# Performance work log

Measured on AMD Instinct MI355X. Metric: run time of the kernel, lower is better.

Reference implementation:

```python
import jax, jax.numpy as jnp
import numpy as np

N = 50000
E = 600000
IN_DIM = 128
HID = 128
HEADS = 4
OUT = HID // HEADS  # per-head out channels
R = 2
LAYERS = 2
NEG_SLOPE = 0.2


def _glorot(key, shape):
    fan_in, fan_out = shape[-2], shape[-1]
    lim = jnp.sqrt(6.0 / (fan_in + fan_out))
    return jax.random.uniform(key, shape, jnp.float32, -lim, lim)


def setup_inputs() -> dict:
    key = jax.random.key(0)
    ks = jax.random.split(key, 20)
    x = jax.random.normal(ks[0], (N, IN_DIM), jnp.float32)
    eidx = jax.random.randint(ks[1], (2, E), 0, N, jnp.int64 if jax.config.jax_enable_x64 else jnp.int32)
    etype = jax.random.randint(ks[2], (E,), 0, R, eidx.dtype)
    d = IN_DIM
    params = {}
    ki = 3
    for l in range(LAYERS):
        params[f"W{l}"] = _glorot(ks[ki], (R, d, HID)); ki += 1            # per-relation weight
        params[f"Q{l}"] = _glorot(ks[ki], (HID, HEADS)); ki += 1           # query proj (dim=1)
        params[f"K{l}"] = _glorot(ks[ki], (HID, HEADS)); ki += 1           # key proj
        params[f"cb{l}"] = jnp.zeros((HID,), jnp.float32)                   # conv bias
        params[f"pW{l}"] = _glorot(ks[ki], (HID, HID)); ki += 1            # proj Linear weight [out,in]
        params[f"pb{l}"] = jnp.zeros((HID,), jnp.float32)
        d = HID
    return dict(x=x, eidx=eidx, etype=etype, **params)


def _rgat_conv(h, src, dst, etype, W, Q, K, b):
    # per-relation transform of all nodes: [R, N, HID]
    xw = jnp.einsum('ni,rio->rno', h, W)
    out_j = xw[etype, src]          # [E, HID] source features under edge's relation
    out_i = xw[etype, dst]          # [E, HID] target features under edge's relation
    # additive self-attention, dim=1: alpha [E, HEADS]
    alpha = jax.nn.leaky_relu(out_i @ Q + out_j @ K, NEG_SLOPE)
    # segment softmax over destination nodes (across-relation)
    m = jax.ops.segment_max(alpha, dst, num_segments=N)
    m = jnp.where(jnp.isfinite(m), m, 0.0)
    e = jnp.exp(alpha - m[dst])
    s = jax.ops.segment_sum(e, dst, num_segments=N)
    a = e / (s[dst] + 1e-16)
    # weighted messages and scatter-sum aggregation
    msg = out_j.reshape(E, HEADS, OUT) * a[:, :, None]
    agg = jax.ops.segment_sum(msg.reshape(E, HID), dst, num_segments=N)
    return agg + b


def reference(x, eidx, etype, W0, Q0, K0, cb0, pW0, pb0, W1, Q1, K1, cb1, pW1, pb1):
    src, dst = eidx[0], eidx[1]  # flow source_to_target: aggregate at eidx[1]
    h = x
    for (W, Q, K, cb, pW, pb) in ((W0, Q0, K0, cb0, pW0, pb0), (W1, Q1, K1, cb1, pW1, pb1)):
        h = _rgat_conv(h, src, dst, etype, W, Q, K, cb)
        h = jax.nn.elu(h @ pW.T + pb)
    return h
```

## Files before the change

kernel.cpp:

```cpp
#include <hip/hip_runtime.h>
#include <hip/hip_bf16.h>

typedef __hip_bfloat16 bf16;
typedef short s16x8 __attribute__((ext_vector_type(8)));
typedef float f32x4 __attribute__((ext_vector_type(4)));

#define N_NODES 50000
#define NPAD    50048
#define E_EDGES 600000
#define HID     128
#define HEADS   4
#define SCAN_B  196

#define GB_IDX  2344
#define GB_XB   3125
#define GB_WT   256
#define GB_QUAD 3125
#define GB_BIG  8824
#define GB_GEMM 1564
#define GB_QK   196

__device__ __forceinline__ unsigned short f2bf_bits(float f) {
  unsigned u = __float_as_uint(f);
  u += 0x7fffu + ((u >> 16) & 1u);
  return (unsigned short)(u >> 16);
}
__device__ __forceinline__ float bf2f(unsigned short b) {
  return __uint_as_float(((unsigned)b) << 16);
}
__device__ __forceinline__ float lo_f(unsigned v) { return __uint_as_float(v << 16); }
__device__ __forceinline__ float hi_f(unsigned v) { return __uint_as_float(v & 0xffff0000u); }
__device__ __forceinline__ float lrelu(float v) { return fmaxf(v, 0.2f * v); }
__device__ __forceinline__ float elu(float v) { return v > 0.f ? v : __expf(v) - 1.f; }

__global__ __launch_bounds__(256) void detect_zero_kernel(const unsigned short* __restrict__ xb,
                                                          const int* __restrict__ ei,
                                                          int* __restrict__ flags,
                                                          int* __restrict__ zp, int nz) {
  int t = threadIdx.x;
  int i = blockIdx.x * 256 + t;
  if (i < nz) zp[i] = 0;
  if (blockIdx.x == 0) {
    __shared__ int cnt[2];
    if (t < 2) cnt[t] = 0;
    __syncthreads();
    unsigned short v = xb[2 * t];
    int ex = (v >> 7) & 0xFF;
    if (ex < 119 || ex > 135) atomicAdd(&cnt[0], 1);
    if (ei[2 * t + 1] != 0) atomicAdd(&cnt[1], 1);
    __syncthreads();
    if (t == 0) {
      flags[0] = (cnt[0] > 64) ? 1 : 0;
      flags[1] = (cnt[1] == 0) ? 1 : 0;
    }
  }
}

struct P8 { const void* src[8]; int dstoff[8]; int n[8]; };
__global__ __launch_bounds__(256) void cvt_all_kernel(const int* __restrict__ eidx,
                                                      const int* __restrict__ etype,
                                                      int* __restrict__ dstA, int* __restrict__ pk,
                                                      int* __restrict__ deg,
                                                      const void* __restrict__ x,
                                                      unsigned short* __restrict__ hb,
                                                      const void* __restrict__ w0,
                                                      const void* __restrict__ w1,
                                                      unsigned short* __restrict__ Wbt,
                                                      P8 tab, float* __restrict__ base,
                                                      const int* __restrict__ flags) {
  const int b = blockIdx.x, t = threadIdx.x;
  if (b < GB_IDX) {
    int e = b * 256 + t;
    if (e >= E_EDGES) return;
    int s, d, r;
    if (flags[1]) {
      const long long* e64 = (const long long*)eidx;
      const long long* t64 = (const long long*)etype;
      s = (int)e64[e]; d = (int)e64[E_EDGES + e]; r = (int)t64[e];
    } else {
      s = eidx[e]; d = eidx[E_EDGES + e]; r = etype[e];
    }
    dstA[e] = d;
    pk[e] = s | (r << 16);
    atomicAdd(&deg[d], 1);
  } else if (b < GB_IDX + GB_XB) {
    int i = (b - GB_IDX) * 256 + t;
    if (flags[0]) {
      const float4* s4 = (const float4*)x;
      float4 a = s4[2 * i], c = s4[2 * i + 1];
      s16x8 o;
      o[0] = (short)f2bf_bits(a.x); o[1] = (short)f2bf_bits(a.y);
      o[2] = (short)f2bf_bits(a.z); o[3] = (short)f2bf_bits(a.w);
      o[4] = (short)f2bf_bits(c.x); o[5] = (short)f2bf_bits(c.y);
      o[6] = (short)f2bf_bits(c.z); o[7] = (short)f2bf_bits(c.w);
      *(s16x8*)(hb + (size_t)i * 8) = o;
    } else {
      *(s16x8*)(hb + (size_t)i * 8) = ((const s16x8*)x)[i];
    }
  } else if (b < GB_IDX + GB_XB + GB_WT) {
    int idx = (b - GB_IDX - GB_XB) * 256 + t;
    int l = idx >> 15, rem = idx & 32767;
    int r = rem >> 14, i = (rem >> 7) & 127, o = rem & 127;
    const void* src = l ? w1 : w0;
    unsigned short v;
    if (flags[0]) v = f2bf_bits(((const float*)src)[rem]);
    else          v = ((const unsigned short*)src)[rem];
    Wbt[(size_t)l * 2 * HID * HID + ((size_t)r * HID + o) * HID + i] = v;
  } else {
    const int f = flags[0];
    int bb = b - GB_IDX - GB_XB - GB_WT;
    for (int k = 0; k < 8; ++k) {
      int n = tab.n[k];
      for (int i = bb * 256 + t; i < n; i += 2 * 256) {
        float v = f ? ((const float*)tab.src[k])[i] : bf2f(((const unsigned short*)tab.src[k])[i]);
        base[tab.dstoff[k] + i] = v;
      }
    }
  }
}

__global__ __launch_bounds__(256) void scan1_bucket_kernel(const int* __restrict__ deg,
                                                           int* __restrict__ excl,
                                                           int* __restrict__ bsum,
                                                           int* __restrict__ bcnt,
                                                           int* __restrict__ nq,
                                                           int* __restrict__ nw) {
  const int b = blockIdx.x, t = threadIdx.x;
  if (b < SCAN_B) {
    __shared__ int sm[256];
    int i = b * 256 + t;
    int v = (i < NPAD) ? deg[i] : 0;
    sm[t] = v;
    __syncthreads();
#pragma unroll
    for (int off = 1; off < 256; off <<= 1) {
      int add = (t >= off) ? sm[t - off] : 0;
      __syncthreads();
      sm[t] += add;
      __syncthreads();
    }
    if (i < NPAD) excl[i] = sm[t] - v;
    if (t == 255) bsum[b] = sm[255];
  } else {
    int n = (b - SCAN_B) * 256 + t;
    int lane = t & 63;
    bool valid = n < N_NODES;
    int d = valid ? deg[n] : 0;
    bool isq = valid && (d <= 16);
    bool isw = valid && (d > 16);
    unsigned long long mq = __ballot(isq);
    unsigned long long mw = __ballot(isw);
    unsigned long long lower = (lane == 63) ? 0x7fffffffffffffffull : ((1ull << lane) - 1ull);
    int baseq = 0, basew = 0;
    int lq = (int)__ffsll(mq) - 1;
    int lw = (int)__ffsll(mw) - 1;
    if (mq && lane == lq) baseq = atomicAdd(&bcnt[0], (int)__popcll(mq));
    if (mw && lane == lw) basew = atomicAdd(&bcnt[1], (int)__popcll(mw));
    if (mq) baseq = __shfl(baseq, lq);
    if (mw) basew = __shfl(basew, lw);
    if (isq) nq[baseq + (int)__popcll(mq & lower)] = n;
    if (isw) nw[basew + (int)__popcll(mw & lower)] = n;
  }
}

__global__ __launch_bounds__(256) void scan23_prep_kernel(const int* __restrict__ excl,
                                                          const int* __restrict__ bsum,
                                                          int* __restrict__ rowstart,
                                                          const unsigned short* __restrict__ Wbt,
                                                          const float* __restrict__ Qf,
                                                          const float* __restrict__ Kf,
                                                          unsigned short* __restrict__ qkt_hi,
                                                          unsigned short* __restrict__ qkt_lo,
                                                          const void* __restrict__ pW0,
                                                          const void* __restrict__ pW1,
                                                          const float* __restrict__ cbf,
                                                          const float* __restrict__ pbf,
                                                          unsigned short* __restrict__ pWTb2,
                                                          float* __restrict__ bo2,
                                                          const int* __restrict__ flags) {
  const int b = blockIdx.x, t = threadIdx.x;
  if (b < SCAN_B) {
    __shared__ int sm[256];
    int v = (t < SCAN_B) ? bsum[t] : 0;
    sm[t] = v;
    __syncthreads();
#pragma unroll
    for (int off = 1; off < 256; off <<= 1) {
      int add = (t >= off) ? sm[t - off] : 0;
      __syncthreads();
      sm[t] += add;
      __syncthreads();
    }
    int bpre = (b > 0) ? sm[b - 1] : 0;
    int i = b * 256 + t;
    if (i < NPAD) rowstart[i] = excl[i] + bpre;
    if (i == 0) rowstart[NPAD] = E_EDGES;
  } else if (b < SCAN_B + 2) {
    int idx = (b - SCAN_B) * 256 + t;
    int i = idx & 127, lr = idx >> 7, l = lr >> 1, r = (lr & 1);
    float aq[4] = {0.f, 0.f, 0.f, 0.f}, ak[4] = {0.f, 0.f, 0.f, 0.f};
    const unsigned short* Wb = Wbt + (size_t)lr * HID * HID;
    const float* Qp = Qf + l * HID * HEADS;
    const float* Kp = Kf + l * HID * HEADS;
    for (int j = 0; j < HID; ++j) {
      float w = bf2f(Wb[j * HID + i]);
      float4 q4 = *(const float4*)(Qp + j * 4);
      float4 k4 = *(const float4*)(Kp + j * 4);
      aq[0] += w * q4.x; aq[1] += w * q4.y; aq[2] += w * q4.z; aq[3] += w * q4.w;
      ak[0] += w * k4.x; ak[1] += w * k4.y; ak[2] += w * k4.z; ak[3] += w * k4.w;
    }
    size_t base = (size_t)l * 16 * HID;
#pragma unroll
    for (int h = 0; h < 4; ++h) {
      unsigned short qh = f2bf_bits(aq[h]);
      unsigned short kh = f2bf_bits(ak[h]);
      float qres = aq[h] - bf2f(qh);
      float kres = ak[h] - bf2f(kh);
      qkt_hi[base + (size_t)(r * 4 + h) * HID + i] = qh;
      qkt_lo[base + (size_t)(r * 4 + h) * HID + i] = f2bf_bits(qres);
      qkt_hi[base + (size_t)(8 + r * 4 + h) * HID + i] = kh;
      qkt_lo[base + (size_t)(8 + r * 4 + h) * HID + i] = f2bf_bits(kres);
    }
  } else {
    const int wave = t >> 6, lane = t & 63;
    int ob = (b - SCAN_B - 2) * 4 + wave;
    int o = ob & 127, l = ob >> 7;
    const void* pWraw = l ? pW1 : pW0;
    const float* cb = cbf + l * HID;
    const int f = flags[0];
    float part = 0.f;
#pragma unroll
    for (int i = lane; i < HID; i += 64) {
      float w = f ? ((const float*)pWraw)[o * HID + i] : bf2f(((const unsigned short*)pWraw)[o * HID + i]);
      pWTb2[(size_t)l * HID * HID + o * HID + i] = f2bf_bits(w);
      part += cb[i] * w;
    }
#pragma unroll
    for (int off = 32; off > 0; off >>= 1) part += __shfl_xor(part, off);
    if (lane == 0) bo2[l * HID + o] = pbf[l * HID + o] + part;
  }
}

__global__ __launch_bounds__(256) void scatter_kernel(const int* __restrict__ dstA,
                                                      const int* __restrict__ pk,
                                                      const int* __restrict__ rowstart,
                                                      int* __restrict__ cnt,
                                                      int* __restrict__ eord) {
  int e = blockIdx.x * 256 + threadIdx.x;
  if (e >= E_EDGES) return;
  int d = dstA[e];
  int pos = rowstart[d] + atomicAdd(&cnt[d], 1);
  eord[pos] = pk[e];
}

__global__ __launch_bounds__(256) void gemm_qk_kernel(const unsigned short* __restrict__ hb,
                                                      const unsigned short* __restrict__ Wbt,
                                                      unsigned short* __restrict__ xw,
                                                      const unsigned short* __restrict__ qkt_hi,
                                                      const unsigned short* __restrict__ qkt_lo,
                                                      float4* __restrict__ qi4,
                                                      float4* __restrict__ kj4) {
  __shared__ unsigned short smem[8704];
  const int t = threadIdx.x;
  const int wave = t >> 6, lane = t & 63;
  const int lm = lane & 15, q = lane >> 4;
  if (blockIdx.x < GB_GEMM) {
    unsigned short (*As)[136] = (unsigned short(*)[136])smem;
    const int row0 = blockIdx.x * 32;
    const int r = wave >> 1, colb = (wave & 1) * 64;
    const unsigned short* Bt = Wbt + (size_t)r * HID * HID;
    s16x8 bfr[4][4];
#pragma unroll
    for (int kc = 0; kc < 4; ++kc) {
      const int ko = kc * 32 + q * 8;
#pragma unroll
      for (int ct = 0; ct < 4; ++ct)
        bfr[kc][ct] = *(const s16x8*)(Bt + (size_t)(colb + ct * 16 + lm) * HID + ko);
    }
    const unsigned short* gsrc = hb + (size_t)row0 * HID;
#pragma unroll
    for (int j = 0; j < 2; ++j) {
      int idx = j * 256 + t;
      *(s16x8*)&As[idx >> 4][(idx & 15) * 8] = *(const s16x8*)(gsrc + idx * 8);
    }
    __syncthreads();
    f32x4 acc[2][4];
#pragma unroll
    for (int a = 0; a < 2; ++a)
#pragma unroll
      for (int c = 0; c < 4; ++c) { f32x4 z = {0.f, 0.f, 0.f, 0.f}; acc[a][c] = z; }
#pragma unroll
    for (int kc = 0; kc < 4; ++kc) {
      const int ko = kc * 32 + q * 8;
#pragma unroll
      for (int rt = 0; rt < 2; ++rt) {
        s16x8 a = *(const s16x8*)&As[rt * 16 + lm][ko];
#pragma unroll
        for (int ct = 0; ct < 4; ++ct)
          acc[rt][ct] = __builtin_amdgcn_mfma_f32_16x16x32_bf16(a, bfr[kc][ct], acc[rt][ct], 0, 0, 0);
      }
    }
    __syncthreads();
#pragma unroll
    for (int rr = 0; rr < 2; ++rr) {
      if (r == rr) {
#pragma unroll
        for (int rt = 0; rt < 2; ++rt)
#pragma unroll
          for (int i = 0; i < 4; ++i) {
            int rloc = rt * 16 + q * 4 + i;
#pragma unroll
            for (int ct = 0; ct < 4; ++ct)
              As[rloc][colb + ct * 16 + lm] = f2bf_bits(acc[rt][ct][i]);
          }
      }
      __syncthreads();
      unsigned short* dst = xw + ((size_t)rr * NPAD + row0) * HID;
#pragma unroll
      for (int j = 0; j < 2; ++j) {
        int idx = j * 256 + t;
        int rw = idx >> 4, cb8 = (idx & 15) * 8;
        if (row0 + rw < N_NODES)
          *(s16x8*)(dst + (size_t)rw * HID + cb8) = *(const s16x8*)&As[rw][cb8];
      }
      __syncthreads();
    }
  } else {
    float (*st)[16][68] = (float(*)[16][68])smem;
    const int row0 = (blockIdx.x - GB_GEMM) * 256 + wave * 64;
    if (row0 < NPAD) {
      s16x8 bhi[4], blo[4], af[4][4];
#pragma unroll
      for (int kc = 0; kc < 4; ++kc) {
        const int ko = kc * 32 + q * 8;
        bhi[kc] = *(const s16x8*)(qkt_hi + (size_t)lm * HID + ko);
        blo[kc] = *(const s16x8*)(qkt_lo + (size_t)lm * HID + ko);
      }
#pragma unroll
      for (int kc = 0; kc < 4; ++kc) {
        const int ko = kc * 32 + q * 8;
#pragma unroll
        for (int rt = 0; rt < 4; ++rt)
          af[kc][rt] = *(const s16x8*)(hb + (size_t)(row0 + rt * 16 + lm) * HID + ko);
      }
      f32x4 acc[4];
#pragma unroll
      for (int a = 0; a < 4; ++a) { f32x4 z = {0.f, 0.f, 0.f, 0.f}; acc[a] = z; }
#pragma unroll
      for (int kc = 0; kc < 4; ++kc)
#pragma unroll
        for (int rt = 0; rt < 4; ++rt) {
          acc[rt] = __builtin_amdgcn_mfma_f32_16x16x32_bf16(af[kc][rt], bhi[kc], acc[rt], 0, 0, 0);
          acc[rt] = __builtin_amdgcn_mfma_f32_16x16x32_bf16(af[kc][rt], blo[kc], acc[rt], 0, 0, 0);
        }
#pragma unroll
      for (int rt = 0; rt < 4; ++rt)
        *(f32x4*)&st[wave][lm][rt * 16 + q * 4] = acc[rt];
    }
    __syncthreads();
    if (row0 < NPAD) {
      int n = row0 + lane;
      if (n < N_NODES) {
        float4 v;
        v.x = st[wave][0][lane]; v.y = st[wave][1][lane]; v.z = st[wave][2][lane]; v.w = st[wave][3][lane];
        qi4[n] = v;
        v.x = st[wave][4][lane]; v.y = st[wave][5][lane]; v.z = st[wave][6][lane]; v.w = st[wave][7][lane];
        qi4[NPAD + n] = v;
        v.x = st[wave][8][lane]; v.y = st[wave][9][lane]; v.z = st[wave][10][lane]; v.w = st[wave][11][lane];
        kj4[n] = v;
        v.x = st[wave][12][lane]; v.y = st[wave][13][lane]; v.z = st[wave][14][lane]; v.w = st[wave][15][lane];
        kj4[NPAD + n] = v;
      }
    }
  }
}

__global__ __launch_bounds__(256) void edge_all_kernel(
    const int* __restrict__ rowstart, const int* __restrict__ eord,
    const float4* __restrict__ qi4, const float4* __restrict__ kj4,
    const unsigned short* __restrict__ xw, unsigned short* __restrict__ aggb,
    const int* __restrict__ nq, const int* __restrict__ nw,
    const int* __restrict__ bcnt) {
  __shared__ volatile float wbuf[1152];
  const int t = threadIdx.x;
  const int wave = t >> 6, lane = t & 63;
  if (blockIdx.x < GB_QUAD) {
    const int g = lane >> 4, li = lane & 15;
    const int idx = blockIdx.x * 16 + wave * 4 + g;
    const int cq = bcnt[0];
    const bool act = idx < cq;
    const int n = act ? nq[idx] : 0;
    const int start = rowstart[n];
    const int dg = act ? (rowstart[n + 1] - start) : 0;
    int p = 0;
    float w0 = 0.f, w1 = 0.f, w2 = 0.f, w3 = 0.f;
    if (li < dg) {
      p = eord[start + li];
      int s = p & 0xffff, r = p >> 16;
      float4 k4 = kj4[r ? (NPAD + s) : s];
      float4 q4 = r ? qi4[NPAD + n] : qi4[n];
      w0 = __expf(fminf(lrelu(q4.x + k4.x), 85.f));
      w1 = __expf(fminf(lrelu(q4.y + k4.y), 85.f));
      w2 = __expf(fminf(lrelu(q4.z + k4.z), 85.f));
      w3 = __expf(fminf(lrelu(q4.w + k4.w), 85.f));
    }
    const int wg = (wave << 2) | g;
    volatile float* wls = &wbuf[wg * 68];
    wls[0 * 17 + li] = w0; wls[1 * 17 + li] = w1;
    wls[2 * 17 + li] = w2; wls[3 * 17 + li] = w3;
    float s0 = w0, s1 = w1, s2 = w2, s3 = w3;
#pragma unroll
    for (int off = 8; off > 0; off >>= 1) {
      s0 += __shfl_xor(s0, off); s1 += __shfl_xor(s1, off);
      s2 += __shfl_xor(s2, off); s3 += __shfl_xor(s3, off);
    }
    const int hh = li >> 2;
    float ssel = hh == 0 ? s0 : hh == 1 ? s1 : hh == 2 ? s2 : s3;
    float a0 = 0.f, a1 = 0.f, a2 = 0.f, a3 = 0.f, a4 = 0.f, a5 = 0.f, a6 = 0.f, a7 = 0.f;
    volatile const float* wrh = &wls[hh * 17];
    const int co = li * 8;
    const int gbase = lane & 48;
#pragma unroll 1
    for (int e0 = 0; e0 < dg; e0 += 4) {
      int pe[4];
      uint4 v[4];
#pragma unroll
      for (int u = 0; u < 4; ++u) {
        int e = e0 + u;
        pe[u] = __shfl(p, gbase + (e < dg ? e : 0));
      }
#pragma unroll
      for (int u = 0; u < 4; ++u)
        v[u] = *(const uint4*)(xw + ((size_t)((pe[u] & 0xffff) + (pe[u] >> 16) * NPAD) << 7) + co);
#pragma unroll
      for (int u = 0; u < 4; ++u) {
        int e = e0 + u;
        float we = (e < dg) ? wrh[e] : 0.f;
        a0 = fmaf(lo_f(v[u].x), we, a0); a1 = fmaf(hi_f(v[u].x), we, a1);
        a2 = fmaf(lo_f(v[u].y), we, a2); a3 = fmaf(hi_f(v[u].y), we, a3);
        a4 = fmaf(lo_f(v[u].z), we, a4); a5 = fmaf(hi_f(v[u].z), we, a5);
        a6 = fmaf(lo_f(v[u].w), we, a6); a7 = fmaf(hi_f(v[u].w), we, a7);
      }
    }
    if (act) {
      float inv = 1.f / (ssel + 1e-16f);
      uint4 o;
      o.x = (unsigned)f2bf_bits(a0 * inv) | ((unsigned)f2bf_bits(a1 * inv) << 16);
      o.y = (unsigned)f2bf_bits(a2 * inv) | ((unsigned)f2bf_bits(a3 * inv) << 16);
      o.z = (unsigned)f2bf_bits(a4 * inv) | ((unsigned)f2bf_bits(a5 * inv) << 16);
      o.w = (unsigned)f2bf_bits(a6 * inv) | ((unsigned)f2bf_bits(a7 * inv) << 16);
      *(uint4*)(aggb + ((size_t)n << 7) + co) = o;
    }
  } else {
    const int idx = (blockIdx.x - GB_QUAD) * 4 + wave;
    const int cw = bcnt[1];
    if (idx >= cw) return;
    const int n = nw[idx];
    unsigned* outp = (unsigned*)(aggb + ((size_t)n << 7)) + lane;
    const int start = rowstart[n];
    const int deg = rowstart[n + 1] - start;
    const int hh = lane >> 4;
    const int ch2 = lane << 1;
    float2 acc = {0.f, 0.f};
    float ssel;
    volatile float* wls = &wbuf[wave * 288];
    if (deg <= 64) {
      int p = 0;
      float w0 = 0.f, w1 = 0.f, w2 = 0.f, w3 = 0.f;
      if (lane < deg) {
        p = eord[start + lane];
        int s = p & 0xffff, r = p >> 16;
        float4 k4 = kj4[r ? (NPAD + s) : s];
        float4 q4 = r ? qi4[NPAD + n] : qi4[n];
        w0 = __expf(fminf(lrelu(q4.x + k4.x), 85.f));
        w1 = __expf(fminf(lrelu(q4.y + k4.y), 85.f));
        w2 = __expf(fminf(lrelu(q4.z + k4.z), 85.f));
        w3 = __expf(fminf(lrelu(q4.w + k4.w), 85.f));
      }
      float s0 = w0, s1 = w1, s2 = w2, s3 = w3;
#pragma unroll
      for (int off = 32; off > 0; off >>= 1) {
        s0 += __shfl_xor(s0, off); s1 += __shfl_xor(s1, off);
        s2 += __shfl_xor(s2, off); s3 += __shfl_xor(s3, off);
      }
      ssel = hh == 0 ? s0 : hh == 1 ? s1 : hh == 2 ? s2 : s3;
      wls[0 * 72 + lane] = w0;
      wls[1 * 72 + lane] = w1;
      wls[2 * 72 + lane] = w2;
      wls[3 * 72 + lane] = w3;
      volatile const float* wrh = &wls[hh * 72];
      const int degp = (deg + 15) & ~15;
#pragma unroll 1
      for (int e = 0; e < degp; e += 16) {
        int pp[16];
        unsigned vv[16];
#pragma unroll
        for (int u = 0; u < 16; ++u)
          pp[u] = __builtin_amdgcn_readlane(p, e + u);
#pragma unroll
        for (int u = 0; u < 16; ++u)
          vv[u] = *(const unsigned*)(xw + ((size_t)((pp[u] & 0xffff) + (pp[u] >> 16) * NPAD) << 7) + ch2);
#pragma unroll
        for (int u = 0; u < 16; ++u) {
          float we = wrh[e + u];
          acc.x = fmaf(lo_f(vv[u]), we, acc.x);
          acc.y = fmaf(hi_f(vv[u]), we, acc.y);
        }
      }
    } else {
      const float4 q0 = qi4[n], q1 = qi4[NPAD + n];
      float4 m = make_float4(-1e30f, -1e30f, -1e30f, -1e30f);
      for (int e = start; e < start + deg; ++e) {
        int pe = eord[e];
        int s = pe & 0xffff, r = pe >> 16;
        float4 k4 = kj4[(size_t)r * NPAD + s];
        float4 q4 = r ? q1 : q0;
        m.x = fmaxf(m.x, lrelu(q4.x + k4.x)); m.y = fmaxf(m.y, lrelu(q4.y + k4.y));
        m.z = fmaxf(m.z, lrelu(q4.z + k4.z)); m.w = fmaxf(m.w, lrelu(q4.w + k4.w));
      }
      float4 sv = make_float4(0.f, 0.f, 0.f, 0.f);
      for (int e = start; e < start + deg; ++e) {
        int pe = eord[e];
        int s = pe & 0xffff, r = pe >> 16;
        float4 k4 = kj4[(size_t)r * NPAD + s];
        float4 q4 = r ? q1 : q0;
        float w0 = __expf(lrelu(q4.x + k4.x) - m.x);
        float w1 = __expf(lrelu(q4.y + k4.y) - m.y);
        float w2 = __expf(lrelu(q4.z + k4.z) - m.z);
        float w3 = __expf(lrelu(q4.w + k4.w) - m.w);
        sv.x += w0; sv.y += w1; sv.z += w2; sv.w += w3;
        float we = hh == 0 ? w0 : hh == 1 ? w1 : hh == 2 ? w2 : w3;
        unsigned v = *(const unsigned*)(xw + (((size_t)r * NPAD + s) << 7) + ch2);
        acc.x = fmaf(lo_f(v), we, acc.x);
        acc.y = fmaf(hi_f(v), we, acc.y);
      }
      ssel = hh == 0 ? sv.x : hh == 1 ? sv.y : hh == 2 ? sv.z : sv.w;
    }
    float inv = 1.f / (ssel + 1e-16f);
    *outp = (unsigned)f2bf_bits(acc.x * inv) | ((unsigned)f2bf_bits(acc.y * inv) << 16);
  }
}

__global__ __launch_bounds__(256) void proj_mfma(const unsigned short* __restrict__ aggb,
                                                 const unsigned short* __restrict__ pWTb,
                                                 const float* __restrict__ bo,
                                                 unsigned short* __restrict__ hbout,
                                                 void* __restrict__ dout,
                                                 const int* __restrict__ flags) {
  __shared__ unsigned short As[64][136];
  const int t = threadIdx.x;
  const int wave = t >> 6, lane = t & 63;
  const int row0 = blockIdx.x * 64;
  const int h = wave >> 1;
  const int colb = (wave & 1) * 64;
  const int lm = lane & 15, q = lane >> 4;
  s16x8 bfr[4][4];
#pragma unroll
  for (int kc = 0; kc < 4; ++kc) {
    const int ko = kc * 32 + q * 8;
#pragma unroll
    for (int ct = 0; ct < 4; ++ct)
      bfr[kc][ct] = *(const s16x8*)(pWTb + (size_t)(colb + ct * 16 + lm) * HID + ko);
  }
  const unsigned short* gsrc = aggb + (size_t)row0 * HID;
#pragma unroll
  for (int j = 0; j < 4; ++j) {
    int idx = j * 256 + t;
    *(s16x8*)&As[idx >> 4][(idx & 15) * 8] = *(const s16x8*)(gsrc + idx * 8);
  }
  __syncthreads();
  f32x4 acc[2][4];
#pragma unroll
  for (int a = 0; a < 2; ++a)
#pragma unroll
    for (int c = 0; c < 4; ++c) { f32x4 z = {0.f, 0.f, 0.f, 0.f}; acc[a][c] = z; }
#pragma unroll
  for (int kc = 0; kc < 4; ++kc) {
    const int ko = kc * 32 + q * 8;
#pragma unroll
    for (int rt = 0; rt < 2; ++rt) {
      s16x8 a = *(const s16x8*)&As[(2 * h + rt) * 16 + lm][ko];
#pragma unroll
      for (int ct = 0; ct < 4; ++ct)
        acc[rt][ct] = __builtin_amdgcn_mfma_f32_16x16x32_bf16(a, bfr[kc][ct], acc[rt][ct], 0, 0, 0);
    }
  }
  __syncthreads();
  const int f32final = (dout != nullptr) && flags[0];
  if (!f32final) {
    unsigned short* dstp = dout ? (unsigned short*)dout : hbout;
#pragma unroll
    for (int rt = 0; rt < 2; ++rt)
#pragma unroll
      for (int i = 0; i < 4; ++i) {
        int rloc = (2 * h + rt) * 16 + q * 4 + i;
#pragma unroll
        for (int ct = 0; ct < 4; ++ct) {
          int o = colb + ct * 16 + lm;
          float v = elu(acc[rt][ct][i] + bo[o]);
          As[rloc][o] = f2bf_bits(v);
        }
      }
    __syncthreads();
#pragma unroll
    for (int j = 0; j < 4; ++j) {
      int idx = j * 256 + t;
      int rw = idx >> 4, cb8 = (idx & 15) * 8;
      if (row0 + rw < N_NODES)
        *(s16x8*)(dstp + (size_t)(row0 + rw) * HID + cb8) = *(const s16x8*)&As[rw][cb8];
    }
  } else {
    float* fdst = (float*)dout;
    float (*Fs)[132] = (float(*)[132])&As[0][0];
#pragma unroll
    for (int h2 = 0; h2 < 2; ++h2) {
      if (h == h2) {
#pragma unroll
        for (int rt = 0; rt < 2; ++rt)
#pragma unroll
          for (int i = 0; i < 4; ++i) {
            int rloc = rt * 16 + q * 4 + i;
#pragma unroll
            for (int ct = 0; ct < 4; ++ct) {
              int o = colb + ct * 16 + lm;
              Fs[rloc][o] = elu(acc[rt][ct][i] + bo[o]);
            }
          }
      }
      __syncthreads();
#pragma unroll
      for (int j = 0; j < 4; ++j) {
        int idx = j * 256 + t;
        int rw = idx >> 5, cb4 = (idx & 31) * 4;
        if (row0 + h2 * 32 + rw < N_NODES)
          *(float4*)(fdst + (size_t)(row0 + h2 * 32 + rw) * HID + cb4) = *(const float4*)&Fs[rw][cb4];
      }
      __syncthreads();
    }
  }
}

extern "C" void kernel_launch(void* const* d_in, const int* in_sizes, int n_in,
                              void* d_out, int out_size, void* d_ws, size_t ws_size,
                              hipStream_t stream) {
  const void* x     = d_in[0];
  const int*  eidx  = (const int*)d_in[1];
  const int*  etype = (const int*)d_in[2];
  const int iW[2] = {3, 9}, iQ[2] = {4, 10}, iK[2] = {5, 11}, icb[2] = {6, 12}, ipW[2] = {7, 13}, ipb[2] = {8, 14};

  float* ws = (float*)d_ws;
  size_t off = 0;
  int*   flags = (int*)(ws + off); off += 16;
  unsigned short* hb   = (unsigned short*)(ws + off); off += (size_t)NPAD * HID / 2;
  unsigned short* xw   = (unsigned short*)(ws + off); off += (size_t)NPAD * HID;
  float* qi   = ws + off; off += (size_t)2 * NPAD * HEADS;
  float* kj   = ws + off; off += (size_t)2 * NPAD * HEADS;
  unsigned short* aggb = (unsigned short*)(ws + off); off += (size_t)NPAD * HID / 2;
  int* dstA = (int*)(ws + off); off += E_EDGES;
  int* pk   = (int*)(ws + off); off += E_EDGES;
  int* eord = (int*)(ws + off); off += E_EDGES;
  int* deg  = (int*)(ws + off); off += NPAD;
  int* cnt  = (int*)(ws + off); off += NPAD;
  int* bcnt = (int*)(ws + off); off += 16;
  int* excl = (int*)(ws + off); off += NPAD;
  int* rowstart = (int*)(ws + off); off += NPAD + 16;
  int* bsum  = (int*)(ws + off); off += 256;
  int* nq   = (int*)(ws + off); off += NPAD;
  int* nwl  = (int*)(ws + off); off += NPAD;
  unsigned short* Wbt   = (unsigned short*)(ws + off); off += (size_t)2 * 2 * HID * HID / 2;
  unsigned short* pWTb2 = (unsigned short*)(ws + off); off += (size_t)2 * HID * HID / 2;
  unsigned short* qkt_hi = (unsigned short*)(ws + off); off += (size_t)2 * 16 * HID / 2;
  unsigned short* qkt_lo = (unsigned short*)(ws + off); off += (size_t)2 * 16 * HID / 2;
  float* Qf  = ws + off; off += 2 * HID * HEADS;
  float* Kf  = ws + off; off += 2 * HID * HEADS;
  float* cbf = ws + off; off += 2 * HID;
  float* pbf = ws + off; off += 2 * HID;
  float* bo2 = ws + off; off += 2 * HID;

  detect_zero_kernel<<<(2 * NPAD + 16 + 255) / 256, 256, 0, stream>>>((const unsigned short*)x, eidx, flags, deg, 2 * NPAD + 16);

  {
    P8 tab;
    float* base = ws;
    for (int l = 0; l < 2; ++l) {
      tab.src[l * 4 + 0] = d_in[iQ[l]];  tab.dstoff[l * 4 + 0] = (int)(Qf - base) + l * HID * HEADS;  tab.n[l * 4 + 0] = HID * HEADS;
      tab.src[l * 4 + 1] = d_in[iK[l]];  tab.dstoff[l * 4 + 1] = (int)(Kf - base) + l * HID * HEADS;  tab.n[l * 4 + 1] = HID * HEADS;
      tab.src[l * 4 + 2] = d_in[icb[l]]; tab.dstoff[l * 4 + 2] = (int)(cbf - base) + l * HID;         tab.n[l * 4 + 2] = HID;
      tab.src[l * 4 + 3] = d_in[ipb[l]]; tab.dstoff[l * 4 + 3] = (int)(pbf - base) + l * HID;         tab.n[l * 4 + 3] = HID;
    }
    cvt_all_kernel<<<GB_IDX + GB_XB + GB_WT + 2, 256, 0, stream>>>(eidx, etype, dstA, pk, deg,
                                                                   x, hb, d_in[iW[0]], d_in[iW[1]], Wbt,
                                                                   tab, ws, flags);
  }

  scan1_bucket_kernel<<<SCAN_B + SCAN_B, 256, 0, stream>>>(deg, excl, bsum, bcnt, nq, nwl);

  scan23_prep_kernel<<<SCAN_B + 2 + 64, 256, 0, stream>>>(excl, bsum, rowstart,
                                                          Wbt, Qf, Kf, qkt_hi, qkt_lo,
                                                          d_in[ipW[0]], d_in[ipW[1]], cbf, pbf, pWTb2, bo2, flags);

  scatter_kernel<<<(E_EDGES + 255) / 256, 256, 0, stream>>>(dstA, pk, rowstart, cnt, eord);

  for (int l = 0; l < 2; ++l) {
    gemm_qk_kernel<<<GB_GEMM + GB_QK, 256, 0, stream>>>(hb, Wbt + (size_t)l * 2 * HID * HID, xw,
                                                        qkt_hi + (size_t)l * 16 * HID, qkt_lo + (size_t)l * 16 * HID,
                                                        (float4*)qi, (float4*)kj);
    edge_all_kernel<<<GB_QUAD + GB_BIG, 256, 0, stream>>>(rowstart, eord, (const float4*)qi, (const float4*)kj,
                                                          xw, aggb, nq, nwl, bcnt);
    proj_mfma<<<NPAD / 64, 256, 0, stream>>>(aggb, pWTb2 + (size_t)l * HID * HID, bo2 + l * HID, hb,
                                             (l == 1) ? d_out : nullptr, flags);
  }
}
```

Baseline: 343.6 us.

## Fuse input conversion and projection into per-layer GEMM+QK kernels

The x-to-bf16 conversion moves out of cvt_all and into a new layer-0 kernel that does the relation GEMM and the Q/K projection from one LDS tile. The layer-0 output projection plus ELU is fused with the layer-1 GEMM and QK, so the intermediate hb buffer is never written to or reread from global memory. The edge kernel's block order is also swapped so the big-node blocks are scheduled first. The goal is fewer launches and less global traffic, at the cost of larger 64-row tiles with two LDS buffers, which may reduce occupancy.

Result: no change. 343.1 us (-0.1%).

```diff
diff --git a/kernel.cpp b/kernel.cpp
--- a/kernel.cpp
+++ b/kernel.cpp
@@ -13,12 +13,9 @@
 #define SCAN_B  196
 
 #define GB_IDX  2344
-#define GB_XB   3125
 #define GB_WT   256
 #define GB_QUAD 3125
 #define GB_BIG  8824
-#define GB_GEMM 1564
-#define GB_QK   196
 
 __device__ __forceinline__ unsigned short f2bf_bits(float f) {
   unsigned u = __float_as_uint(f);
@@ -61,8 +58,6 @@
                                                       const int* __restrict__ etype,
                                                       int* __restrict__ dstA, int* __restrict__ pk,
                                                       int* __restrict__ deg,
-                                                      const void* __restrict__ x,
-                                                      unsigned short* __restrict__ hb,
                                                       const void* __restrict__ w0,
                                                       const void* __restrict__ w1,
                                                       unsigned short* __restrict__ Wbt,
@@ -83,22 +78,8 @@
     dstA[e] = d;
     pk[e] = s | (r << 16);
     atomicAdd(&deg[d], 1);
-  } else if (b < GB_IDX + GB_XB) {
-    int i = (b - GB_IDX) * 256 + t;
-    if (flags[0]) {
-      const float4* s4 = (const float4*)x;
-      float4 a = s4[2 * i], c = s4[2 * i + 1];
-      s16x8 o;
-      o[0] = (short)f2bf_bits(a.x); o[1] = (short)f2bf_bits(a.y);
-      o[2] = (short)f2bf_bits(a.z); o[3] = (short)f2bf_bits(a.w);
-      o[4] = (short)f2bf_bits(c.x); o[5] = (short)f2bf_bits(c.y);
-      o[6] = (short)f2bf_bits(c.z); o[7] = (short)f2bf_bits(c.w);
-      *(s16x8*)(hb + (size_t)i * 8) = o;
-    } else {
-      *(s16x8*)(hb + (size_t)i * 8) = ((const s16x8*)x)[i];
-    }
-  } else if (b < GB_IDX + GB_XB + GB_WT) {
-    int idx = (b - GB_IDX - GB_XB) * 256 + t;
+  } else if (b < GB_IDX + GB_WT) {
+    int idx = (b - GB_IDX) * 256 + t;
     int l = idx >> 15, rem = idx & 32767;
     int r = rem >> 14, i = (rem >> 7) & 127, o = rem & 127;
     const void* src = l ? w1 : w0;
@@ -108,7 +89,7 @@
     Wbt[(size_t)l * 2 * HID * HID + ((size_t)r * HID + o) * HID + i] = v;
   } else {
     const int f = flags[0];
-    int bb = b - GB_IDX - GB_XB - GB_WT;
+    int bb = b - GB_IDX - GB_WT;
     for (int k = 0; k < 8; ++k) {
       int n = tab.n[k];
       for (int i = bb * 256 + t; i < n; i += 2 * 256) {
@@ -253,126 +234,214 @@
   eord[pos] = pk[e];
 }
 
-__global__ __launch_bounds__(256) void gemm_qk_kernel(const unsigned short* __restrict__ hb,
-                                                      const unsigned short* __restrict__ Wbt,
-                                                      unsigned short* __restrict__ xw,
-                                                      const unsigned short* __restrict__ qkt_hi,
-                                                      const unsigned short* __restrict__ qkt_lo,
-                                                      float4* __restrict__ qi4,
-                                                      float4* __restrict__ kj4) {
-  __shared__ unsigned short smem[8704];
+__device__ __forceinline__ void gemm64_from_lds(unsigned short (*As)[136], unsigned short (*Cs)[136],
+                                                const unsigned short* __restrict__ Wbt,
+                                                unsigned short* __restrict__ xw, int row0,
+                                                int wave, int lm, int q, int t) {
+  const int r = wave >> 1, colb = (wave & 1) * 64;
+  const unsigned short* Bt = Wbt + (size_t)r * HID * HID;
+  s16x8 bfr[4][4];
+#pragma unroll
+  for (int kc = 0; kc < 4; ++kc) {
+    const int ko = kc * 32 + q * 8;
+#pragma unroll
+    for (int ct = 0; ct < 4; ++ct)
+      bfr[kc][ct] = *(const s16x8*)(Bt + (size_t)(colb + ct * 16 + lm) * HID + ko);
+  }
+  f32x4 acc[4][4];
+#pragma unroll
+  for (int a = 0; a < 4; ++a)
+#pragma unroll
+    for (int c = 0; c < 4; ++c) { f32x4 z = {0.f, 0.f, 0.f, 0.f}; acc[a][c] = z; }
+#pragma unroll
+  for (int kc = 0; kc < 4; ++kc) {
+    const int ko = kc * 32 + q * 8;
+#pragma unroll
+    for (int rt = 0; rt < 4; ++rt) {
+      s16x8 a = *(const s16x8*)&As[rt * 16 + lm][ko];
+#pragma unroll
+      for (int ct = 0; ct < 4; ++ct)
+        acc[rt][ct] = __builtin_amdgcn_mfma_f32_16x16x32_bf16(a, bfr[kc][ct], acc[rt][ct], 0, 0, 0);
+    }
+  }
+  __syncthreads();
+#pragma unroll
+  for (int rr = 0; rr < 2; ++rr) {
+    if (r == rr) {
+#pragma unroll
+      for (int rt = 0; rt < 4; ++rt)
+#pragma unroll
+        for (int i = 0; i < 4; ++i) {
+          int rloc = rt * 16 + q * 4 + i;
+#pragma unroll
+          for (int ct = 0; ct < 4; ++ct)
+            Cs[rloc][colb + ct * 16 + lm] = f2bf_bits(acc[rt][ct][i]);
+        }
+    }
+    __syncthreads();
+    unsigned short* dst = xw + ((size_t)rr * NPAD + row0) * HID;
+#pragma unroll
+    for (int j = 0; j < 4; ++j) {
+      int idx = j * 256 + t;
+      int rw = idx >> 4, cb8 = (idx & 15) * 8;
+      if (row0 + rw < N_NODES)
+        *(s16x8*)(dst + (size_t)rw * HID + cb8) = *(const s16x8*)&Cs[rw][cb8];
+    }
+    __syncthreads();
+  }
+}
+
+__device__ __forceinline__ void qk16_from_lds(unsigned short (*As)[136], unsigned short (*Cs)[136],
+                                              const unsigned short* __restrict__ qkt_hi,
+                                              const unsigned short* __restrict__ qkt_lo,
+                                              float4* __restrict__ qi4, float4* __restrict__ kj4,
+                                              int row0, int wave, int lane, int lm, int q) {
+  s16x8 bhi[4], blo[4], af[4];
+#pragma unroll
+  for (int kc = 0; kc < 4; ++kc) {
+    const int ko = kc * 32 + q * 8;
+    bhi[kc] = *(const s16x8*)(qkt_hi + (size_t)lm * HID + ko);
+    blo[kc] = *(const s16x8*)(qkt_lo + (size_t)lm * HID + ko);
+    af[kc]  = *(const s16x8*)&As[wave * 16 + lm][ko];
+  }
+  f32x4 acc = {0.f, 0.f, 0.f, 0.f};
+#pragma unroll
+  for (int kc = 0; kc < 4; ++kc) {
+    acc = __builtin_amdgcn_mfma_f32_16x16x32_bf16(af[kc], bhi[kc], acc, 0, 0, 0);
+    acc = __builtin_amdgcn_mfma_f32_16x16x32_bf16(af[kc], blo[kc], acc, 0, 0, 0);
+  }
+  float (*Fs)[16][17] = (float(*)[16][17])&Cs[0][0];
+#pragma unroll
+  for (int i = 0; i < 4; ++i)
+    Fs[wave][lm][q * 4 + i] = acc[i];
+  __syncthreads();
+  if (lane < 16) {
+    int n = row0 + wave * 16 + lane;
+    if (n < N_NODES) {
+      float4 v;
+      v.x = Fs[wave][0][lane];  v.y = Fs[wave][1][lane];  v.z = Fs[wave][2][lane];  v.w = Fs[wave][3][lane];
+      qi4[n] = v;
+      v.x = Fs[wave][4][lane];  v.y = Fs[wave][5][lane];  v.z = Fs[wave][6][lane];  v.w = Fs[wave][7][lane];
+      qi4[NPAD + n] = v;
+      v.x = Fs[wave][8][lane];  v.y = Fs[wave][9][lane];  v.z = Fs[wave][10][lane]; v.w = Fs[wave][11][lane];
+      kj4[n] = v;
+      v.x = Fs[wave][12][lane]; v.y = Fs[wave][13][lane]; v.z = Fs[wave][14][lane]; v.w = Fs[wave][15][lane];
+      kj4[NPAD + n] = v;
+    }
+  }
+}
+
+__global__ __launch_bounds__(256) void fused_l0_kernel(const void* __restrict__ x,
+                                                       const unsigned short* __restrict__ Wbt,
+                                                       unsigned short* __restrict__ xw,
+                                                       const unsigned short* __restrict__ qkt_hi,
+                                                       const unsigned short* __restrict__ qkt_lo,
+                                                       float4* __restrict__ qi4,
+                                                       float4* __restrict__ kj4,
+                                                       const int* __restrict__ flags) {
+  __shared__ unsigned short As[64][136];
+  __shared__ unsigned short Cs[64][136];
   const int t = threadIdx.x;
   const int wave = t >> 6, lane = t & 63;
   const int lm = lane & 15, q = lane >> 4;
-  if (blockIdx.x < GB_GEMM) {
-    unsigned short (*As)[136] = (unsigned short(*)[136])smem;
-    const int row0 = blockIdx.x * 32;
-    const int r = wave >> 1, colb = (wave & 1) * 64;
-    const unsigned short* Bt = Wbt + (size_t)r * HID * HID;
-    s16x8 bfr[4][4];
-#pragma unroll
-    for (int kc = 0; kc < 4; ++kc) {
-      const int ko = kc * 32 + q * 8;
+  const int row0 = blockIdx.x * 64;
+  if (flags[0]) {
+    const float* xf = (const float*)x;
+#pragma unroll
+    for (int j = 0; j < 4; ++j) {
+      int idx = j * 256 + t;
+      int rw = idx >> 4, cb8 = (idx & 15) * 8;
+      s16x8 o = {0, 0, 0, 0, 0, 0, 0, 0};
+      if (row0 + rw < N_NODES) {
+        const float4* s4 = (const float4*)(xf + (size_t)(row0 + rw) * HID + cb8);
+        float4 a = s4[0], b = s4[1];
+        o[0] = (short)f2bf_bits(a.x); o[1] = (short)f2bf_bits(a.y);
+        o[2] = (short)f2bf_bits(a.z); o[3] = (short)f2bf_bits(a.w);
+        o[4] = (short)f2bf_bits(b.x); o[5] = (short)f2bf_bits(b.y);
+        o[6] = (short)f2bf_bits(b.z); o[7] = (short)f2bf_bits(b.w);
+      }
+      *(s16x8*)&As[rw][cb8] = o;
+    }
+  } else {
+    const unsigned short* xb = (const unsigned short*)x;
+#pragma unroll
+    for (int j = 0; j < 4; ++j) {
+      int idx = j * 256 + t;
+      int rw = idx >> 4, cb8 = (idx & 15) * 8;
+      s16x8 o = {0, 0, 0, 0, 0, 0, 0, 0};
+      if (row0 + rw < N_NODES)
+        o = *(const s16x8*)(xb + (size_t)(row0 + rw) * HID + cb8);
+      *(s16x8*)&As[rw][cb8] = o;
+    }
+  }
+  __syncthreads();
+  gemm64_from_lds(As, Cs, Wbt, xw, row0, wave, lm, q, t);
+  qk16_from_lds(As, Cs, qkt_hi, qkt_lo, qi4, kj4, row0, wave, lane, lm, q);
+}
+
+__global__ __launch_bounds__(256) void fused_mid_kernel(const unsigned short* __restrict__ aggb,
+                                                        const unsigned short* __restrict__ pWTb,
+                                                        const float* __restrict__ bo,
+                                                        const unsigned short* __restrict__ Wbt1,
+                                                        unsigned short* __restrict__ xw,
+                                                        const unsigned short* __restrict__ qkt_hi,
+                                                        const unsigned short* __restrict__ qkt_lo,
+                                                        float4* __restrict__ qi4,
+                                                        float4* __restrict__ kj4) {
+  __shared__ unsigned short As[64][136];
+  __shared__ unsigned short Cs[64][136];
+  const int t = threadIdx.x;
+  const int wave = t >> 6, lane = t & 63;
+  const int lm = lane & 15, q = lane >> 4;
+  const int row0 = blockIdx.x * 64;
+  const int h = wave >> 1;
+  const int colb = (wave & 1) * 64;
+  s16x8 bfr[4][4];
+#pragma unroll
+  for (int kc = 0; kc < 4; ++kc) {
+    const int ko = kc * 32 + q * 8;
+#pragma unroll
+    for (int ct = 0; ct < 4; ++ct)
+      bfr[kc][ct] = *(const s16x8*)(pWTb + (size_t)(colb + ct * 16 + lm) * HID + ko);
+  }
+  const unsigned short* gsrc = aggb + (size_t)row0 * HID;
+#pragma unroll
+  for (int j = 0; j < 4; ++j) {
+    int idx = j * 256 + t;
+    *(s16x8*)&As[idx >> 4][(idx & 15) * 8] = *(const s16x8*)(gsrc + idx * 8);
+  }
+  __syncthreads();
+  f32x4 pacc[2][4];
+#pragma unroll
+  for (int a = 0; a < 2; ++a)
+#pragma unroll
+    for (int c = 0; c < 4; ++c) { f32x4 z = {0.f, 0.f, 0.f, 0.f}; pacc[a][c] = z; }
+#pragma unroll
+  for (int kc = 0; kc < 4; ++kc) {
+    const int ko = kc * 32 + q * 8;
+#pragma unroll
+    for (int rt = 0; rt < 2; ++rt) {
+      s16x8 a = *(const s16x8*)&As[(2 * h + rt) * 16 + lm][ko];
 #pragma unroll
       for (int ct = 0; ct < 4; ++ct)
-        bfr[kc][ct] = *(const s16x8*)(Bt + (size_t)(colb + ct * 16 + lm) * HID + ko);
-    }
-    const unsigned short* gsrc = hb + (size_t)row0 * HID;
-#pragma unroll
-    for (int j = 0; j < 2; ++j) {
-      int idx = j * 256 + t;
-      *(s16x8*)&As[idx >> 4][(idx & 15) * 8] = *(const s16x8*)(gsrc + idx * 8);
-    }
-    __syncthreads();
-    f32x4 acc[2][4];
-#pragma unroll
-    for (int a = 0; a < 2; ++a)
-#pragma unroll
-      for (int c = 0; c < 4; ++c) { f32x4 z = {0.f, 0.f, 0.f, 0.f}; acc[a][c] = z; }
-#pragma unroll
-    for (int kc = 0; kc < 4; ++kc) {
-      const int ko = kc * 32 + q * 8;
-#pragma unroll
-      for (int rt = 0; rt < 2; ++rt) {
-        s16x8 a = *(const s16x8*)&As[rt * 16 + lm][ko];
-#pragma unroll
-        for (int ct = 0; ct < 4; ++ct)
-          acc[rt][ct] = __builtin_amdgcn_mfma_f32_16x16x32_bf16(a, bfr[kc][ct], acc[rt][ct], 0, 0, 0);
-      }
-    }
-    __syncthreads();
-#pragma unroll
-    for (int rr = 0; rr < 2; ++rr) {
-      if (r == rr) {
-#pragma unroll
-        for (int rt = 0; rt < 2; ++rt)
-#pragma unroll
-          for (int i = 0; i < 4; ++i) {
-            int rloc = rt * 16 + q * 4 + i;
-#pragma unroll
-            for (int ct = 0; ct < 4; ++ct)
-              As[rloc][colb + ct * 16 + lm] = f2bf_bits(acc[rt][ct][i]);
-          }
-      }
-      __syncthreads();
-      unsigned short* dst = xw + ((size_t)rr * NPAD + row0) * HID;
-#pragma unroll
-      for (int j = 0; j < 2; ++j) {
-        int idx = j * 256 + t;
-        int rw = idx >> 4, cb8 = (idx & 15) * 8;
-        if (row0 + rw < N_NODES)
-          *(s16x8*)(dst + (size_t)rw * HID + cb8) = *(const s16x8*)&As[rw][cb8];
-      }
-      __syncthreads();
-    }
-  } else {
-    float (*st)[16][68] = (float(*)[16][68])smem;
-    const int row0 = (blockIdx.x - GB_GEMM) * 256 + wave * 64;
-    if (row0 < NPAD) {
-      s16x8 bhi[4], blo[4], af[4][4];
-#pragma unroll
-      for (int kc = 0; kc < 4; ++kc) {
-        const int ko = kc * 32 + q * 8;
-        bhi[kc] = *(const s16x8*)(qkt_hi + (size_t)lm * HID + ko);
-        blo[kc] = *(const s16x8*)(qkt_lo + (size_t)lm * HID + ko);
-      }
-#pragma unroll
-      for (int kc = 0; kc < 4; ++kc) {
-        const int ko = kc * 32 + q * 8;
-#pragma unroll
-        for (int rt = 0; rt < 4; ++rt)
-          af[kc][rt] = *(const s16x8*)(hb + (size_t)(row0 + rt * 16 + lm) * HID + ko);
-      }
-      f32x4 acc[4];
-#pragma unroll
-      for (int a = 0; a < 4; ++a) { f32x4 z = {0.f, 0.f, 0.f, 0.f}; acc[a] = z; }
-#pragma unroll
-      for (int kc = 0; kc < 4; ++kc)
-#pragma unroll
-        for (int rt = 0; rt < 4; ++rt) {
-          acc[rt] = __builtin_amdgcn_mfma_f32_16x16x32_bf16(af[kc][rt], bhi[kc], acc[rt], 0, 0, 0);
-          acc[rt] = __builtin_amdgcn_mfma_f32_16x16x32_bf16(af[kc][rt], blo[kc], acc[rt], 0, 0, 0);
-        }
-#pragma unroll
-      for (int rt = 0; rt < 4; ++rt)
-        *(f32x4*)&st[wave][lm][rt * 16 + q * 4] = acc[rt];
-    }
-    __syncthreads();
-    if (row0 < NPAD) {
-      int n = row0 + lane;
-      if (n < N_NODES) {
-        float4 v;
-        v.x = st[wave][0][lane]; v.y = st[wave][1][lane]; v.z = st[wave][2][lane]; v.w = st[wave][3][lane];
-        qi4[n] = v;
-        v.x = st[wave][4][lane]; v.y = st[wave][5][lane]; v.z = st[wave][6][lane]; v.w = st[wave][7][lane];
-        qi4[NPAD + n] = v;
-        v.x = st[wave][8][lane]; v.y = st[wave][9][lane]; v.z = st[wave][10][lane]; v.w = st[wave][11][lane];
-        kj4[n] = v;
-        v.x = st[wave][12][lane]; v.y = st[wave][13][lane]; v.z = st[wave][14][lane]; v.w = st[wave][15][lane];
-        kj4[NPAD + n] = v;
-      }
-    }
-  }
+        pacc[rt][ct] = __builtin_amdgcn_mfma_f32_16x16x32_bf16(a, bfr[kc][ct], pacc[rt][ct], 0, 0, 0);
+    }
+  }
+  __syncthreads();
+#pragma unroll
+  for (int rt = 0; rt < 2; ++rt)
+#pragma unroll
+    for (int i = 0; i < 4; ++i) {
+      int rloc = (2 * h + rt) * 16 + q * 4 + i;
+#pragma unroll
+      for (int ct = 0; ct < 4; ++ct) {
+        int o = colb + ct * 16 + lm;
+        As[rloc][o] = f2bf_bits(elu(pacc[rt][ct][i] + bo[o]));
+      }
+    }
+  __syncthreads();
+  gemm64_from_lds(As, Cs, Wbt1, xw, row0, wave, lm, q, t);
+  qk16_from_lds(As, Cs, qkt_hi, qkt_lo, qi4, kj4, row0, wave, lane, lm, q);
 }
 
 __global__ __launch_bounds__(256) void edge_all_kernel(
@@ -384,9 +453,9 @@
   __shared__ volatile float wbuf[1152];
   const int t = threadIdx.x;
   const int wave = t >> 6, lane = t & 63;
-  if (blockIdx.x < GB_QUAD) {
+  if (blockIdx.x >= GB_BIG) {
     const int g = lane >> 4, li = lane & 15;
-    const int idx = blockIdx.x * 16 + wave * 4 + g;
+    const int idx = (blockIdx.x - GB_BIG) * 16 + wave * 4 + g;
     const int cq = bcnt[0];
     const bool act = idx < cq;
     const int n = act ? nq[idx] : 0;
@@ -452,7 +521,7 @@
       *(uint4*)(aggb + ((size_t)n << 7) + co) = o;
     }
   } else {
-    const int idx = (blockIdx.x - GB_QUAD) * 4 + wave;
+    const int idx = blockIdx.x * 4 + wave;
     const int cw = bcnt[1];
     if (idx >= cw) return;
     const int n = nw[idx];
@@ -541,12 +610,11 @@
   }
 }
 
-__global__ __launch_bounds__(256) void proj_mfma(const unsigned short* __restrict__ aggb,
-                                                 const unsigned short* __restrict__ pWTb,
-                                                 const float* __restrict__ bo,
-                                                 unsigned short* __restrict__ hbout,
-                                                 void* __restrict__ dout,
-                                                 const int* __restrict__ flags) {
+__global__ __launch_bounds__(256) void proj_final(const unsigned short* __restrict__ aggb,
+                                                  const unsigned short* __restrict__ pWTb,
+                                                  const float* __restrict__ bo,
+                                                  void* __restrict__ dout,
+                                                  const int* __restrict__ flags) {
   __shared__ unsigned short As[64][136];
   const int t = threadIdx.x;
   const int wave = t >> 6, lane = t & 63;
@@ -586,9 +654,8 @@
     }
   }
   __syncthreads();
-  const int f32final = (dout != nullptr) && flags[0];
-  if (!f32final) {
-    unsigned short* dstp = dout ? (unsigned short*)dout : hbout;
+  if (!flags[0]) {
+    unsigned short* dstp = (unsigned short*)dout;
 #pragma unroll
     for (int rt = 0; rt < 2; ++rt)
 #pragma unroll
@@ -597,8 +664,7 @@
 #pragma unroll
         for (int ct = 0; ct < 4; ++ct) {
           int o = colb + ct * 16 + lm;
-          float v = elu(acc[rt][ct][i] + bo[o]);
-          As[rloc][o] = f2bf_bits(v);
+          As[rloc][o] = f2bf_bits(elu(acc[rt][ct][i] + bo[o]));
         }
       }
     __syncthreads();
@@ -651,7 +717,6 @@
   float* ws = (float*)d_ws;
   size_t off = 0;
   int*   flags = (int*)(ws + off); off += 16;
-  unsigned short* hb   = (unsigned short*)(ws + off); off += (size_t)NPAD * HID / 2;
   unsigned short* xw   = (unsigned short*)(ws + off); off += (size_t)NPAD * HID;
   float* qi   = ws + off; off += (size_t)2 * NPAD * HEADS;
   float* kj   = ws + off; off += (size_t)2 * NPAD * HEADS;
@@ -688,9 +753,9 @@
       tab.src[l * 4 + 2] = d_in[icb[l]]; tab.dstoff[l * 4 + 2] = (int)(cbf - base) + l * HID;         tab.n[l * 4 + 2] = HID;
       tab.src[l * 4 + 3] = d_in[ipb[l]]; tab.dstoff[l * 4 + 3] = (int)(pbf - base) + l * HID;         tab.n[l * 4 + 3] = HID;
     }
-    cvt_all_kernel<<<GB_IDX + GB_XB + GB_WT + 2, 256, 0, stream>>>(eidx, etype, dstA, pk, deg,
-                                                                   x, hb, d_in[iW[0]], d_in[iW[1]], Wbt,
-                                                                   tab, ws, flags);
+    cvt_all_kernel<<<GB_IDX + GB_WT + 2, 256, 0, stream>>>(eidx, etype, dstA, pk, deg,
+                                                           d_in[iW[0]], d_in[iW[1]], Wbt,
+                                                           tab, ws, flags);
   }
 
   scan1_bucket_kernel<<<SCAN_B + SCAN_B, 256, 0, stream>>>(deg, excl, bsum, bcnt, nq, nwl);
@@ -701,13 +766,15 @@
 
   scatter_kernel<<<(E_EDGES + 255) / 256, 256, 0, stream>>>(dstA, pk, rowstart, cnt, eord);
 
-  for (int l = 0; l < 2; ++l) {
-    gemm_qk_kernel<<<GB_GEMM + GB_QK, 256, 0, stream>>>(hb, Wbt + (size_t)l * 2 * HID * HID, xw,
-                                                        qkt_hi + (size_t)l * 16 * HID, qkt_lo + (size_t)l * 16 * HID,
-                                                        (float4*)qi, (float4*)kj);
-    edge_all_kernel<<<GB_QUAD + GB_BIG, 256, 0, stream>>>(rowstart, eord, (const float4*)qi, (const float4*)kj,
-                                                          xw, aggb, nq, nwl, bcnt);
-    proj_mfma<<<NPAD / 64, 256, 0, stream>>>(aggb, pWTb2 + (size_t)l * HID * HID, bo2 + l * HID, hb,
-                                             (l == 1) ? d_out : nullptr, flags);
-  }
-}
+  const int RB = NPAD / 64;
+  fused_l0_kernel<<<RB, 256, 0, stream>>>(x, Wbt, xw, qkt_hi, qkt_lo,
+                                          (float4*)qi, (float4*)kj, flags);
+  edge_all_kernel<<<GB_BIG + GB_QUAD, 256, 0, stream>>>(rowstart, eord, (const float4*)qi, (const float4*)kj,
+                                                        xw, aggb, nq, nwl, bcnt);
+  fused_mid_kernel<<<RB, 256, 0, stream>>>(aggb, pWTb2, bo2, Wbt + (size_t)2 * HID * HID, xw,
+                                           qkt_hi + (size_t)16 * HID, qkt_lo + (size_t)16 * HID,
+                                           (float4*)qi, (float4*)kj);
+  edge_all_kernel<<<GB_BIG + GB_QUAD, 256, 0, stream>>>(rowstart, eord, (const float4*)qi, (const float4*)kj,
+                                                        xw, aggb, nq, nwl, bcnt);
+  proj_final<<<RB, 256, 0, stream>>>(aggb, pWTb2 + (size_t)HID * HID, bo2 + HID, d_out, flags);
+}
```
